# Performance work log

Measured on AMD Instinct MI355X. Metric: run time of the kernel, lower is better.

The kernel has to match this reference:

```python
import jax, jax.numpy as jnp
import numpy as np

TOP_K = 10  # hardcoded k in the original tf.math.top_k call
EPS = 1e-8


def _make_boxes(key, n):
    # valid xyxy boxes in a ~1024x1024 image
    k1, k2 = jax.random.split(key)
    xy = jax.random.uniform(k1, (n, 2), dtype=jnp.float32) * 900.0
    wh = jax.random.uniform(k2, (n, 2), dtype=jnp.float32) * 120.0 + 4.0
    return jnp.concatenate([xy, xy + wh], axis=-1)


def _pairwise_iou(a, b):
    # a: [N,4] xyxy, b: [M,4] xyxy -> [N,M]
    lt = jnp.maximum(a[:, None, :2], b[None, :, :2])  # [N,M,2]
    rb = jnp.minimum(a[:, None, 2:], b[None, :, 2:])  # [N,M,2]
    wh = jnp.clip(rb - lt, 0.0)
    inter = wh[..., 0] * wh[..., 1]                    # [N,M]
    area_a = (a[:, 2] - a[:, 0]) * (a[:, 3] - a[:, 1])  # [N]
    area_b = (b[:, 2] - b[:, 0]) * (b[:, 3] - b[:, 1])  # [M]
    union = area_a[:, None] + area_b[None, :] - inter
    return inter / (union + EPS)


def setup_inputs() -> dict:
    key = jax.random.key(0)
    k1, k2, k3, k4 = jax.random.split(key, 4)
    N, M, C = 16384, 2048, 81
    proposals = _make_boxes(k1, N)
    gt_proposals = _make_boxes(k2, M)
    cls_prob = jax.random.uniform(k3, (N, C), dtype=jnp.float32)
    gt_cls = jax.random.randint(k4, (M,), 0, C, dtype=jnp.int32)
    return {"proposals": proposals, "cls_prob": cls_prob,
            "gt_proposals": gt_proposals, "gt_cls": gt_cls}


def reference(proposals, cls_prob, gt_proposals, gt_cls):
    # Reachable math of ProposalTargetLayer.call (the original aborts via
    # embed()/exit() right after building the top-k mask `i`).
    iou = _pairwise_iou(proposals, gt_proposals)          # [N,M]
    flat = jnp.reshape(iou, (-1,))
    _, top_idx = jax.lax.top_k(flat, TOP_K)
    # tensor_scatter_nd_update of ones onto a zero tensor -> boolean top-k mask
    mask_flat = jnp.zeros_like(flat).at[top_idx].set(1.0)
    mask = jnp.reshape(mask_flat, iou.shape).astype(jnp.bool_)  # [N,M]
    return (iou, mask)
```

## Files before the change

kernel.cpp:

```cpp
#include <hip/hip_runtime.h>

#define TOPK 10
#define BLK 256
#define ROWS_PER_BLOCK 8
#define CAND_CAP 32768
#define SLACK 2e-5f

typedef float f4vec __attribute__((ext_vector_type(4)));

__device__ __forceinline__ bool better(float v1, int i1, float v2, int i2) {
    return (v1 > v2) || (v1 == v2 && i1 < i2);
}

__device__ __forceinline__ void insert10(float (&lv)[TOPK], int (&li)[TOPK],
                                         float v, int ix, float& mv, int& mi) {
    int ws = 0; float wv = lv[0]; int wi = li[0];
#pragma unroll
    for (int j = 1; j < TOPK; ++j)
        if (better(wv, wi, lv[j], li[j])) { wv = lv[j]; wi = li[j]; ws = j; }
#pragma unroll
    for (int j = 0; j < TOPK; ++j)
        if (j == ws) { lv[j] = v; li[j] = ix; }
    mv = lv[0]; mi = li[0];
#pragma unroll
    for (int j = 1; j < TOPK; ++j)
        if (better(mv, mi, lv[j], li[j])) { mv = lv[j]; mi = li[j]; }
}

__device__ __forceinline__ void waveReduceTop10(float (&lv)[TOPK], int (&li)[TOPK],
                                                float* wcv, int* wci, int tid) {
    const int wave = tid >> 6;
    const int lane = tid & 63;
    for (int r = 0; r < TOPK; ++r) {
        float bv = lv[0]; int bi = li[0];
#pragma unroll
        for (int j = 1; j < TOPK; ++j)
            if (better(lv[j], li[j], bv, bi)) { bv = lv[j]; bi = li[j]; }
#pragma unroll
        for (int off = 32; off >= 1; off >>= 1) {
            float ov = __shfl_xor(bv, off, 64);
            int   oi = __shfl_xor(bi, off, 64);
            if (better(ov, oi, bv, bi)) { bv = ov; bi = oi; }
        }
#pragma unroll
        for (int j = 0; j < TOPK; ++j)
            if (lv[j] == bv && li[j] == bi) { lv[j] = -2.0f; li[j] = 0x7fffffff; }
        if (lane == 0) { wcv[wave * TOPK + r] = bv; wci[wave * TOPK + r] = bi; }
    }
}

template <typename EmitFn>
__device__ __forceinline__ void wave0FinalTop10(const float* wcv, const int* wci,
                                                int tid, EmitFn emit) {
    float v = (tid < 40) ? wcv[tid] : -2.0f;
    int   ix = (tid < 40) ? wci[tid] : 0x7fffffff;
    for (int r = 0; r < TOPK; ++r) {
        float bv = v; int bi = ix;
#pragma unroll
        for (int off = 32; off >= 1; off >>= 1) {
            float ov = __shfl_xor(bv, off, 64);
            int   oi = __shfl_xor(bi, off, 64);
            if (better(ov, oi, bv, bi)) { bv = ov; bi = oi; }
        }
        if (v == bv && ix == bi) { v = -2.0f; ix = 0x7fffffff; }
        if (tid == 0) emit(r, bv, bi);
    }
}

__device__ __forceinline__ float iou_exact(const float4 a, const float aA,
                                           const float4 b, const float bA) {
    const float ltx = fmaxf(a.x, b.x);
    const float lty = fmaxf(a.y, b.y);
    const float rbx = fminf(a.z, b.z);
    const float rby = fminf(a.w, b.w);
    const float w = fmaxf(rbx - ltx, 0.0f);
    const float h = fmaxf(rby - lty, 0.0f);
    const float inter = __fmul_rn(w, h);
    const float s = aA + bA;
    const float uni = s - inter;
    const float den = uni + 1e-8f;
    return inter / den;
}

__device__ __forceinline__ float iou_fast(const float4 a, const float aA,
                                          const float4 b, const float bA) {
    const float ltx = fmaxf(a.x, b.x);
    const float lty = fmaxf(a.y, b.y);
    const float rbx = fminf(a.z, b.z);
    const float rby = fminf(a.w, b.w);
    const float w = fmaxf(rbx - ltx, 0.0f);
    const float h = fmaxf(rby - lty, 0.0f);
    const float inter = w * h;
    const float den = (aA + bA - inter) + 1e-8f;
    return inter * __builtin_amdgcn_rcpf(den);
}

__global__ __launch_bounds__(BLK) void sample_max_kernel(
    const float4* __restrict__ prop, const float4* __restrict__ gt,
    float* __restrict__ blockmax, int N, int M) {
    const int tid = threadIdx.x;
    const int bid = blockIdx.x;
    const int row = bid * ROWS_PER_BLOCK + (tid & 7);
    long long c = ((long long)(tid >> 3) * M) >> 5;
    const int col = (int)((c + (bid & 63)) % M);

    float v = -2.0f;
    if (row < N) {
        const float4 a = prop[row];
        const float aA = (a.z - a.x) * (a.w - a.y);
        const float4 b = gt[col];
        const float bA = (b.z - b.x) * (b.w - b.y);
        v = iou_fast(a, aA, b, bA);
    }

    __shared__ float sred[4];
#pragma unroll
    for (int off = 32; off >= 1; off >>= 1)
        v = fmaxf(v, __shfl_xor(v, off, 64));
    if ((tid & 63) == 0) sred[tid >> 6] = v;
    __syncthreads();
    if (tid == 0)
        blockmax[bid] = fmaxf(fmaxf(sred[0], sred[1]), fmaxf(sred[2], sred[3]));
}

__global__ __launch_bounds__(BLK) void threshold_kernel(
    const float* __restrict__ blockmax, int nb,
    float* __restrict__ tm_ptr, int* __restrict__ cand_cnt) {
    __shared__ float wcv[4 * TOPK];
    __shared__ int   wci[4 * TOPK];
    const int tid = threadIdx.x;

    float lv[TOPK]; int li[TOPK];
#pragma unroll
    for (int j = 0; j < TOPK; ++j) { lv[j] = -2.0f; li[j] = 0x7fffffff; }
    float mv = -2.0f; int mi = 0x7fffffff;

    for (int i = tid; i < nb; i += BLK) {
        const float v = blockmax[i];
        if (better(v, i, mv, mi)) insert10(lv, li, v, i, mv, mi);
    }
    waveReduceTop10(lv, li, wcv, wci, tid);
    __syncthreads();
    if (tid < 64) {
        wave0FinalTop10(wcv, wci, tid, [&](int r, float bv, int bi) {
            (void)bi;
            if (r == TOPK - 1) *tm_ptr = bv - SLACK;
        });
    }
    if (tid == 0) *cand_cnt = 0;
}

__global__ __launch_bounds__(BLK) void iou_main_kernel(
    const float4* __restrict__ prop, const float4* __restrict__ gt,
    float* __restrict__ iou_out, float* __restrict__ mask_out,
    const float* __restrict__ tm_ptr, int* __restrict__ cand_cnt,
    int* __restrict__ cand_idx, int N, int M) {
    const int tid = threadIdx.x;
    const int bid = blockIdx.x;
    const int row0 = bid * ROWS_PER_BLOCK;
    const float Tm = *tm_ptr;
    const int M4 = M & ~3;
    const f4vec zero4 = {0.0f, 0.0f, 0.0f, 0.0f};

    for (int m0 = 4 * tid; m0 < M4; m0 += 4 * BLK) {
        const float4 b0 = gt[m0 + 0], b1 = gt[m0 + 1], b2 = gt[m0 + 2], b3 = gt[m0 + 3];
        const float bA0 = (b0.z - b0.x) * (b0.w - b0.y);
        const float bA1 = (b1.z - b1.x) * (b1.w - b1.y);
        const float bA2 = (b2.z - b2.x) * (b2.w - b2.y);
        const float bA3 = (b3.z - b3.x) * (b3.w - b3.y);
#pragma unroll
        for (int nl = 0; nl < ROWS_PER_BLOCK; ++nl) {
            const int row = row0 + nl;
            if (row < N) {
                const float4 a = prop[row];
                const float aA = (a.z - a.x) * (a.w - a.y);
                const float i0 = iou_fast(a, aA, b0, bA0);
                const float i1 = iou_fast(a, aA, b1, bA1);
                const float i2 = iou_fast(a, aA, b2, bA2);
                const float i3 = iou_fast(a, aA, b3, bA3);
                const long long base = (long long)row * M + m0;
                const f4vec iv = {i0, i1, i2, i3};
                __builtin_nontemporal_store(iv, (f4vec*)(iou_out + base));
                __builtin_nontemporal_store(zero4, (f4vec*)(mask_out + base));
                if (i0 >= Tm || i1 >= Tm || i2 >= Tm || i3 >= Tm) {
                    if (i0 >= Tm) { int s = atomicAdd(cand_cnt, 1); if (s < CAND_CAP) cand_idx[s] = (int)base; }
                    if (i1 >= Tm) { int s = atomicAdd(cand_cnt, 1); if (s < CAND_CAP) cand_idx[s] = (int)base + 1; }
                    if (i2 >= Tm) { int s = atomicAdd(cand_cnt, 1); if (s < CAND_CAP) cand_idx[s] = (int)base + 2; }
                    if (i3 >= Tm) { int s = atomicAdd(cand_cnt, 1); if (s < CAND_CAP) cand_idx[s] = (int)base + 3; }
                }
            }
        }
    }
    for (int m = M4 + tid; m < M; m += BLK) {
        const float4 b = gt[m];
        const float bA = (b.z - b.x) * (b.w - b.y);
#pragma unroll
        for (int nl = 0; nl < ROWS_PER_BLOCK; ++nl) {
            const int row = row0 + nl;
            if (row < N) {
                const float4 a = prop[row];
                const float aA = (a.z - a.x) * (a.w - a.y);
                const float v = iou_fast(a, aA, b, bA);
                const long long idx = (long long)row * M + m;
                iou_out[idx] = v;
                mask_out[idx] = 0.0f;
                if (v >= Tm) { int s = atomicAdd(cand_cnt, 1); if (s < CAND_CAP) cand_idx[s] = (int)idx; }
            }
        }
    }
}

__global__ __launch_bounds__(BLK) void final_kernel(
    const float4* __restrict__ prop, const float4* __restrict__ gt,
    const int* __restrict__ cand_cnt, const int* __restrict__ cand_idx,
    float* __restrict__ mask_out, int M) {
    __shared__ float wcv[4 * TOPK];
    __shared__ int   wci[4 * TOPK];
    const int tid = threadIdx.x;
    int c = *cand_cnt;
    if (c > CAND_CAP) c = CAND_CAP;

    float lv[TOPK]; int li[TOPK];
#pragma unroll
    for (int j = 0; j < TOPK; ++j) { lv[j] = -2.0f; li[j] = 0x7fffffff; }
    float mv = -2.0f; int mi = 0x7fffffff;

    for (int i = tid; i < c; i += BLK) {
        const int idx = cand_idx[i];
        const int row = idx / M;
        const int col = idx - row * M;
        const float4 a = prop[row];
        const float4 b = gt[col];
        const float aA = __fmul_rn(a.z - a.x, a.w - a.y);
        const float bA = __fmul_rn(b.z - b.x, b.w - b.y);
        const float v = iou_exact(a, aA, b, bA);
        if (better(v, idx, mv, mi)) insert10(lv, li, v, idx, mv, mi);
    }
    waveReduceTop10(lv, li, wcv, wci, tid);
    __syncthreads();
    if (tid < 64) {
        wave0FinalTop10(wcv, wci, tid, [&](int r, float bv, int bi) {
            (void)r;
            if (bi >= 0 && bi != 0x7fffffff && bv >= 0.0f) mask_out[bi] = 1.0f;
        });
    }
}

extern "C" void kernel_launch(void* const* d_in, const int* in_sizes, int n_in,
                              void* d_out, int out_size, void* d_ws, size_t ws_size,
                              hipStream_t stream) {
    const float4* prop = (const float4*)d_in[0];
    const float4* gt = (const float4*)d_in[2];
    const int N = in_sizes[0] / 4;
    const int M = in_sizes[2] / 4;

    float* iou_out = (float*)d_out;
    float* mask_out = iou_out + (long long)N * M;

    const int nblocks = (N + ROWS_PER_BLOCK - 1) / ROWS_PER_BLOCK;

    char* ws = (char*)d_ws;
    float* blockmax = (float*)ws;
    float* tm_ptr = (float*)(ws + 16384);
    int* cand_cnt = (int*)(ws + 16388);
    int* cand_idx = (int*)(ws + 16392);

    sample_max_kernel<<<nblocks, BLK, 0, stream>>>(prop, gt, blockmax, N, M);
    threshold_kernel<<<1, BLK, 0, stream>>>(blockmax, nblocks, tm_ptr, cand_cnt);
    iou_main_kernel<<<nblocks, BLK, 0, stream>>>(prop, gt, iou_out, mask_out,
                                                 tm_ptr, cand_cnt, cand_idx, N, M);
    final_kernel<<<1, BLK, 0, stream>>>(prop, gt, cand_cnt, cand_idx, mask_out, M);
}
```

Measured before the change: 102.7 us.

## Replace threshold kernel with atomic slot maxima and split mask zero-fill into own kernel

Drops the single-block threshold kernel. Sample blocks now write their maxima into 10 slots with atomicMax, and the main kernel takes the minimum of those slots as a looser lower bound on the top-10 threshold. The main kernel now handles 16 rows per block with the proposal boxes held in registers, uses plain stores instead of nontemporal ones, and no longer writes the mask. A separate grid-stride kernel zero-fills the mask. This removes a serial launch and reloads of the proposals, but the threshold from 10 bucketed maxima may admit more candidates, and the M%4 tail path is gone, so M must be a multiple of 4.

```diff
diff --git a/kernel.cpp b/kernel.cpp
--- a/kernel.cpp
+++ b/kernel.cpp
@@ -2,9 +2,11 @@
 
 #define TOPK 10
 #define BLK 256
-#define ROWS_PER_BLOCK 8
+#define ROWS_SAMPLE 8
+#define ROWS_MAIN 16
 #define CAND_CAP 32768
 #define SLACK 2e-5f
+#define NSLOTS 10
 
 typedef float f4vec __attribute__((ext_vector_type(4)));
 
@@ -97,14 +99,14 @@
 
 __global__ __launch_bounds__(BLK) void sample_max_kernel(
     const float4* __restrict__ prop, const float4* __restrict__ gt,
-    float* __restrict__ blockmax, int N, int M) {
+    unsigned int* __restrict__ slots, int N, int M) {
     const int tid = threadIdx.x;
     const int bid = blockIdx.x;
-    const int row = bid * ROWS_PER_BLOCK + (tid & 7);
+    const int row = bid * ROWS_SAMPLE + (tid & 7);
     long long c = ((long long)(tid >> 3) * M) >> 5;
     const int col = (int)((c + (bid & 63)) % M);
 
-    float v = -2.0f;
+    float v = 0.0f;
     if (row < N) {
         const float4 a = prop[row];
         const float aA = (a.z - a.x) * (a.w - a.y);
@@ -119,70 +121,55 @@
         v = fmaxf(v, __shfl_xor(v, off, 64));
     if ((tid & 63) == 0) sred[tid >> 6] = v;
     __syncthreads();
-    if (tid == 0)
-        blockmax[bid] = fmaxf(fmaxf(sred[0], sred[1]), fmaxf(sred[2], sred[3]));
-}
-
-__global__ __launch_bounds__(BLK) void threshold_kernel(
-    const float* __restrict__ blockmax, int nb,
-    float* __restrict__ tm_ptr, int* __restrict__ cand_cnt) {
-    __shared__ float wcv[4 * TOPK];
-    __shared__ int   wci[4 * TOPK];
-    const int tid = threadIdx.x;
-
-    float lv[TOPK]; int li[TOPK];
-#pragma unroll
-    for (int j = 0; j < TOPK; ++j) { lv[j] = -2.0f; li[j] = 0x7fffffff; }
-    float mv = -2.0f; int mi = 0x7fffffff;
-
-    for (int i = tid; i < nb; i += BLK) {
-        const float v = blockmax[i];
-        if (better(v, i, mv, mi)) insert10(lv, li, v, i, mv, mi);
-    }
-    waveReduceTop10(lv, li, wcv, wci, tid);
-    __syncthreads();
-    if (tid < 64) {
-        wave0FinalTop10(wcv, wci, tid, [&](int r, float bv, int bi) {
-            (void)bi;
-            if (r == TOPK - 1) *tm_ptr = bv - SLACK;
-        });
-    }
-    if (tid == 0) *cand_cnt = 0;
+    if (tid == 0) {
+        const float bm = fmaxf(fmaxf(sred[0], sred[1]), fmaxf(sred[2], sred[3]));
+        atomicMax(&slots[bid % NSLOTS], __float_as_uint(bm));
+    }
 }
 
 __global__ __launch_bounds__(BLK) void iou_main_kernel(
     const float4* __restrict__ prop, const float4* __restrict__ gt,
-    float* __restrict__ iou_out, float* __restrict__ mask_out,
-    const float* __restrict__ tm_ptr, int* __restrict__ cand_cnt,
+    float* __restrict__ iou_out,
+    const unsigned int* __restrict__ slots, int* __restrict__ cand_cnt,
     int* __restrict__ cand_idx, int N, int M) {
     const int tid = threadIdx.x;
     const int bid = blockIdx.x;
-    const int row0 = bid * ROWS_PER_BLOCK;
-    const float Tm = *tm_ptr;
-    const int M4 = M & ~3;
-    const f4vec zero4 = {0.0f, 0.0f, 0.0f, 0.0f};
-
-    for (int m0 = 4 * tid; m0 < M4; m0 += 4 * BLK) {
-        const float4 b0 = gt[m0 + 0], b1 = gt[m0 + 1], b2 = gt[m0 + 2], b3 = gt[m0 + 3];
+    const int row0 = bid * ROWS_MAIN;
+
+    unsigned int mn = slots[0];
+#pragma unroll
+    for (int s = 1; s < NSLOTS; ++s) mn = min(mn, slots[s]);
+    const float Tm = __uint_as_float(mn) - SLACK;
+
+    float4 pa[ROWS_MAIN];
+    float  paA[ROWS_MAIN];
+#pragma unroll
+    for (int nl = 0; nl < ROWS_MAIN; ++nl) {
+        const int r = row0 + nl;
+        const float4 a = (r < N) ? prop[r] : make_float4(0.f, 0.f, 0.f, 0.f);
+        pa[nl] = a;
+        paA[nl] = (a.z - a.x) * (a.w - a.y);
+    }
+
+    for (int c0 = 4 * tid; c0 < M; c0 += 4 * BLK) {
+        const float4 b0 = gt[c0 + 0], b1 = gt[c0 + 1], b2 = gt[c0 + 2], b3 = gt[c0 + 3];
         const float bA0 = (b0.z - b0.x) * (b0.w - b0.y);
         const float bA1 = (b1.z - b1.x) * (b1.w - b1.y);
         const float bA2 = (b2.z - b2.x) * (b2.w - b2.y);
         const float bA3 = (b3.z - b3.x) * (b3.w - b3.y);
 #pragma unroll
-        for (int nl = 0; nl < ROWS_PER_BLOCK; ++nl) {
+        for (int nl = 0; nl < ROWS_MAIN; ++nl) {
             const int row = row0 + nl;
             if (row < N) {
-                const float4 a = prop[row];
-                const float aA = (a.z - a.x) * (a.w - a.y);
-                const float i0 = iou_fast(a, aA, b0, bA0);
-                const float i1 = iou_fast(a, aA, b1, bA1);
-                const float i2 = iou_fast(a, aA, b2, bA2);
-                const float i3 = iou_fast(a, aA, b3, bA3);
-                const long long base = (long long)row * M + m0;
+                const float i0 = iou_fast(pa[nl], paA[nl], b0, bA0);
+                const float i1 = iou_fast(pa[nl], paA[nl], b1, bA1);
+                const float i2 = iou_fast(pa[nl], paA[nl], b2, bA2);
+                const float i3 = iou_fast(pa[nl], paA[nl], b3, bA3);
+                const long long base = (long long)row * M + c0;
                 const f4vec iv = {i0, i1, i2, i3};
-                __builtin_nontemporal_store(iv, (f4vec*)(iou_out + base));
-                __builtin_nontemporal_store(zero4, (f4vec*)(mask_out + base));
-                if (i0 >= Tm || i1 >= Tm || i2 >= Tm || i3 >= Tm) {
+                *reinterpret_cast<f4vec*>(iou_out + base) = iv;
+                const float mx = fmaxf(fmaxf(i0, i1), fmaxf(i2, i3));
+                if (mx >= Tm) {
                     if (i0 >= Tm) { int s = atomicAdd(cand_cnt, 1); if (s < CAND_CAP) cand_idx[s] = (int)base; }
                     if (i1 >= Tm) { int s = atomicAdd(cand_cnt, 1); if (s < CAND_CAP) cand_idx[s] = (int)base + 1; }
                     if (i2 >= Tm) { int s = atomicAdd(cand_cnt, 1); if (s < CAND_CAP) cand_idx[s] = (int)base + 2; }
@@ -191,23 +178,14 @@
             }
         }
     }
-    for (int m = M4 + tid; m < M; m += BLK) {
-        const float4 b = gt[m];
-        const float bA = (b.z - b.x) * (b.w - b.y);
-#pragma unroll
-        for (int nl = 0; nl < ROWS_PER_BLOCK; ++nl) {
-            const int row = row0 + nl;
-            if (row < N) {
-                const float4 a = prop[row];
-                const float aA = (a.z - a.x) * (a.w - a.y);
-                const float v = iou_fast(a, aA, b, bA);
-                const long long idx = (long long)row * M + m;
-                iou_out[idx] = v;
-                mask_out[idx] = 0.0f;
-                if (v >= Tm) { int s = atomicAdd(cand_cnt, 1); if (s < CAND_CAP) cand_idx[s] = (int)idx; }
-            }
-        }
-    }
+}
+
+__global__ __launch_bounds__(BLK) void mask_fill_kernel(
+    float* __restrict__ mask_out, long long n4) {
+    const f4vec zero4 = {0.0f, 0.0f, 0.0f, 0.0f};
+    const long long stride = (long long)gridDim.x * BLK;
+    for (long long i = (long long)blockIdx.x * BLK + threadIdx.x; i < n4; i += stride)
+        *((f4vec*)mask_out + i) = zero4;
 }
 
 __global__ __launch_bounds__(BLK) void final_kernel(
@@ -257,17 +235,20 @@
     float* iou_out = (float*)d_out;
     float* mask_out = iou_out + (long long)N * M;
 
-    const int nblocks = (N + ROWS_PER_BLOCK - 1) / ROWS_PER_BLOCK;
-
     char* ws = (char*)d_ws;
-    float* blockmax = (float*)ws;
-    float* tm_ptr = (float*)(ws + 16384);
-    int* cand_cnt = (int*)(ws + 16388);
-    int* cand_idx = (int*)(ws + 16392);
-
-    sample_max_kernel<<<nblocks, BLK, 0, stream>>>(prop, gt, blockmax, N, M);
-    threshold_kernel<<<1, BLK, 0, stream>>>(blockmax, nblocks, tm_ptr, cand_cnt);
-    iou_main_kernel<<<nblocks, BLK, 0, stream>>>(prop, gt, iou_out, mask_out,
-                                                 tm_ptr, cand_cnt, cand_idx, N, M);
+    unsigned int* slots = (unsigned int*)ws;
+    int* cand_cnt = (int*)(ws + 40);
+    int* cand_idx = (int*)(ws + 64);
+
+    hipMemsetAsync(ws, 0, 44, stream);
+
+    const int nb_sample = (N + ROWS_SAMPLE - 1) / ROWS_SAMPLE;
+    const int nb_main = (N + ROWS_MAIN - 1) / ROWS_MAIN;
+    const long long n4 = ((long long)N * M) >> 2;
+
+    sample_max_kernel<<<nb_sample, BLK, 0, stream>>>(prop, gt, slots, N, M);
+    iou_main_kernel<<<nb_main, BLK, 0, stream>>>(prop, gt, iou_out, slots,
+                                                 cand_cnt, cand_idx, N, M);
+    mask_fill_kernel<<<2048, BLK, 0, stream>>>(mask_out, n4);
     final_kernel<<<1, BLK, 0, stream>>>(prop, gt, cand_cnt, cand_idx, mask_out, M);
 }
```

Result: slower. 122.0 us (+18.8%).
